# Kernel tuning notes

Measured on AMD Instinct MI355X. Metric: run time of the kernel, lower is better.

The kernel has to match this reference:

```python
import jax, jax.numpy as jnp
import numpy as np

EPS = 1e-5

def _graph_conv(x, src, dst, W, b, N):
    # DGL GraphConv, norm='both': D_out^{-1/2} then aggregate then D_in^{-1/2}
    ones = jnp.ones((src.shape[0],), x.dtype)
    out_deg = jnp.clip(jax.ops.segment_sum(ones, src, num_segments=N), 1.0)
    in_deg = jnp.clip(jax.ops.segment_sum(ones, dst, num_segments=N), 1.0)
    h = (x * (out_deg ** -0.5)[:, None]) @ W          # [N, out] (mult W before gather)
    agg = jax.ops.segment_sum(h[src], dst, num_segments=N)  # [N, out] irregular scatter
    return agg * (in_deg ** -0.5)[:, None] + b

def _bn_relu(h, gamma, beta):
    # BatchNorm1d in training mode: batch stats over node axis (biased var)
    mu = jnp.mean(h, axis=0)
    var = jnp.mean((h - mu) ** 2, axis=0)
    return jax.nn.relu((h - mu) * jax.lax.rsqrt(var + EPS) * gamma + beta)

def setup_inputs() -> dict:
    key = jax.random.key(0)
    ks = jax.random.split(key, 6)
    N, E, F, H, C = 100000, 1000000, 128, 128, 16
    return {
        "x": jax.random.normal(ks[0], (N, F), dtype=jnp.float32),
        "src": jax.random.randint(ks[1], (E,), 0, N, dtype=jnp.int32),
        "dst": jax.random.randint(ks[2], (E,), 0, N, dtype=jnp.int32),
        "W1": jax.random.normal(ks[3], (F, H), dtype=jnp.float32) * 0.05,
        "b1": jnp.zeros((H,), jnp.float32),
        "g1": jnp.ones((H,), jnp.float32),
        "be1": jnp.zeros((H,), jnp.float32),
        "W2": jax.random.normal(ks[4], (H, H), dtype=jnp.float32) * 0.05,
        "b2": jnp.zeros((H,), jnp.float32),
        "g2": jnp.ones((H,), jnp.float32),
        "be2": jnp.zeros((H,), jnp.float32),
        "Wc": jax.random.normal(ks[5], (H, C), dtype=jnp.float32) * 0.05,
        "bc": jnp.zeros((C,), jnp.float32),
    }

def reference(x, src, dst, W1, b1, g1, be1, W2, b2, g2, be2, Wc, bc):
    N = x.shape[0]
    h = _bn_relu(_graph_conv(x, src, dst, W1, b1, N), g1, be1)  # dropout = identity (eval)
    h = _bn_relu(_graph_conv(h, src, dst, W2, b2, N), g2, be2)
    return h @ Wc + bc  # [N, num_cls]
```

## Files before the change

kernel.cpp:

```cpp
#include <hip/hip_runtime.h>

#define FDIM 128
#define MAXDEG 64
#define GATHERB 2048
#define NREP 32

#define RSIZE 128
#define RSHIFT 7
#define RCAP 1024
#define CCAP 14336
#define PCAP 80
#define WCONVB 8

typedef unsigned short ushort_t;
typedef unsigned int uint_t;
typedef __attribute__((ext_vector_type(8))) short short8;
typedef __attribute__((ext_vector_type(16))) float float16;

__device__ __forceinline__ float bflo(uint_t u) { return __uint_as_float(u << 16); }
__device__ __forceinline__ float bfhi(uint_t u) { return __uint_as_float(u & 0xffff0000u); }
__device__ __forceinline__ ushort_t f2bf(float f) {
    uint_t u = __float_as_uint(f);
    return (ushort_t)((u + 0x7fffu + ((u >> 16) & 1u)) >> 16);
}
__device__ __forceinline__ uint_t pack2bf(float lo, float hi) {
    return (uint_t)f2bf(lo) | ((uint_t)f2bf(hi) << 16);
}

__global__ __launch_bounds__(256) void gemm1_kernel(
    const float* __restrict__ x, const ushort_t* __restrict__ wb,
    ushort_t* __restrict__ outb, int N) {
    __shared__ ushort_t zt[64][136];
    __shared__ ushort_t wt[128][136];
    int t = threadIdx.x;
    int base = blockIdx.x * 64;

    const uint4* wb4 = (const uint4*)wb;
    for (int i = t; i < FDIM * 16; i += 256) {
        int n = i >> 4, q = i & 15;
        *(uint4*)&wt[n][q * 8] = wb4[n * 16 + q];
    }
    const float4* x4 = (const float4*)x;
    for (int i = t; i < 64 * 32; i += 256) {
        int row = i >> 5, c4 = i & 31;
        int grow = base + row;
        uint2 o = make_uint2(0u, 0u);
        if (grow < N) {
            float4 v = x4[(size_t)grow * 32 + c4];
            o.x = pack2bf(v.x, v.y);
            o.y = pack2bf(v.z, v.w);
        }
        *(uint2*)&zt[row][c4 * 4] = o;
    }
    __syncthreads();

    int wv = t >> 6, lane = t & 63;
    int rt = wv >> 1;
    int m = lane & 31;
    int kg = lane >> 5;

    short8 af[8];
#pragma unroll
    for (int kk = 0; kk < 8; kk++)
        af[kk] = *(const short8*)&zt[rt * 32 + m][kk * 16 + kg * 8];

#pragma unroll
    for (int cc = 0; cc < 2; cc++) {
        int ct = (wv & 1) * 2 + cc;
        float16 acc = {0, 0, 0, 0, 0, 0, 0, 0, 0, 0, 0, 0, 0, 0, 0, 0};
#pragma unroll
        for (int kk = 0; kk < 8; kk++) {
            short8 bf = *(const short8*)&wt[ct * 32 + m][kk * 16 + kg * 8];
            acc = __builtin_amdgcn_mfma_f32_32x32x16_bf16(af[kk], bf, acc, 0, 0, 0);
        }
        int col = ct * 32 + m;
#pragma unroll
        for (int r = 0; r < 16; r++) {
            int row = base + rt * 32 + (r & 3) + 8 * (r >> 2) + 4 * kg;
            if (row < N) outb[(size_t)row * FDIM + col] = f2bf(acc[r]);
        }
    }
}

__global__ __launch_bounds__(256) void bucket_kernel(
    const int* __restrict__ src, const int* __restrict__ dst,
    uint_t* __restrict__ bktD, int* __restrict__ baseD,
    uint_t* __restrict__ bktS, int* __restrict__ baseS,
    const float* __restrict__ W1, const float* __restrict__ W2,
    ushort_t* __restrict__ wb1, ushort_t* __restrict__ wb2,
    int E, int P, int R) {
    __shared__ uint4 buf4[CCAP / 4];
    __shared__ int hist[RCAP];
    __shared__ int scanbuf[256];
    uint_t* buf = (uint_t*)buf4;
    int t = threadIdx.x;

    if (blockIdx.x >= 2 * P) {
        int t0 = (blockIdx.x - 2 * P) * 256 + t;
        for (int i = t0; i < FDIM * FDIM; i += WCONVB * 256) {
            int k = i >> 7, n = i & 127;
            wb1[n * FDIM + k] = f2bf(W1[i]);
            wb2[n * FDIM + k] = f2bf(W2[i]);
        }
        return;
    }

    int role = blockIdx.x >= P;
    int p = role ? blockIdx.x - P : blockIdx.x;
    const int* key = role ? src : dst;
    int e0 = p * CCAP;
    int e1 = min(E, e0 + CCAP);
    int cnt = e1 - e0;

    for (int r = t; r < R; r += 256) hist[r] = 0;
    __syncthreads();
    for (int i = e0 + t; i < e1; i += 256) atomicAdd(&hist[key[i] >> RSHIFT], 1);
    __syncthreads();

    int b0 = t * 4;
    int hv[4];
    int s0 = 0;
#pragma unroll
    for (int k = 0; k < 4; k++) {
        hv[k] = (b0 + k < R) ? hist[b0 + k] : 0;
        s0 += hv[k];
    }
    scanbuf[t] = s0;
    __syncthreads();
    for (int off = 1; off < 256; off <<= 1) {
        int v = (t >= off) ? scanbuf[t - off] : 0;
        __syncthreads();
        scanbuf[t] += v;
        __syncthreads();
    }
    int run = scanbuf[t] - s0;
    int* baseG = role ? baseS : baseD;
#pragma unroll
    for (int k = 0; k < 4; k++) {
        if (b0 + k < R) {
            baseG[(b0 + k) * P + p] = run;
            hist[b0 + k] = run;
        }
        run += hv[k];
    }
    if (t == 0) baseG[R * P + p] = cnt;
    __syncthreads();

    for (int i = e0 + t; i < e1; i += 256) {
        int kv = key[i];
        int slot = atomicAdd(&hist[kv >> RSHIFT], 1);
        uint_t entry = role ? (uint_t)kv
                            : (((uint_t)(kv & (RSIZE - 1)) << 25) | (uint_t)src[i]);
        buf[slot] = entry;
    }
    __syncthreads();

    uint_t* outp = role ? bktS : bktD;
    uint4* og = (uint4*)(outp + (size_t)e0);
    int n4 = (cnt + 3) >> 2;
    for (int j = t; j < n4; j += 256) og[j] = buf4[j];
}

__global__ __launch_bounds__(256) void build_kernel(
    const uint_t* __restrict__ bktD, const int* __restrict__ baseD,
    const uint_t* __restrict__ bktS, const int* __restrict__ baseS,
    int* __restrict__ eidx, int* __restrict__ cnt, int* __restrict__ cs,
    int N, int P) {
    __shared__ uint4 ell4[RSIZE][MAXDEG / 4];
    __shared__ int cntN[RSIZE], csN[RSIZE];
    __shared__ int dB0[PCAP], dB1[PCAP], sB0[PCAP], sB1[PCAP];
    uint_t* ell = (uint_t*)ell4;
    int t = threadIdx.x;
    int r = blockIdx.x;

    if (t < RSIZE) { cntN[t] = 0; csN[t] = 0; }
    for (int i = t; i < P; i += 256) {
        dB0[i] = baseD[r * P + i];
        dB1[i] = baseD[(r + 1) * P + i];
        sB0[i] = baseS[r * P + i];
        sB1[i] = baseS[(r + 1) * P + i];
    }
    __syncthreads();

    int wave = t >> 6, lane = t & 63;
    for (int p = wave; p < P; p += 4) {
        int b = dB0[p], len = dB1[p] - b;
        const uint_t* seg = bktD + (size_t)p * CCAP + b;
        for (int i = lane; i < len; i += 64) {
            uint_t e = seg[i];
            int dl = e >> 25;
            uint_t s = e & 0x1FFFFFFu;
            int slot = atomicAdd(&cntN[dl], 1);
            if (slot < MAXDEG) ell[dl * MAXDEG + slot] = s;
        }
        int b2 = sB0[p], len2 = sB1[p] - b2;
        const uint_t* seg2 = bktS + (size_t)p * CCAP + b2;
        for (int i = lane; i < len2; i += 64)
            atomicAdd(&csN[seg2[i] & (RSIZE - 1)], 1);
    }
    __syncthreads();

    int base = r * RSIZE;
    for (int i = t; i < RSIZE * (MAXDEG / 4); i += 256) {
        int n = i >> 4, q = i & 15;
        int g = base + n;
        if (g < N && q * 4 < min(cntN[n], MAXDEG))
            ((uint4*)eidx)[(size_t)g * (MAXDEG / 4) + q] = ell4[n][q];
    }
    if (t < RSIZE) {
        int g = base + t;
        if (g < N) { cnt[g] = cntN[t]; cs[g] = csN[t]; }
    }
}

template <bool OS>
__global__ __launch_bounds__(256) void gather_kernel(const ushort_t* __restrict__ hb,
                                                     const int* __restrict__ eidx,
                                                     const int* __restrict__ cnt,
                                                     const int* __restrict__ cs,
                                                     const float* __restrict__ b,
                                                     ushort_t* __restrict__ outb,
                                                     float* __restrict__ statsRep, int N) {
    __shared__ float4 redS[256];
    __shared__ float4 redQ[256];
    int t = threadIdx.x;
    int wave = t >> 6, lane = t & 63;
    int half = lane >> 5, sub = lane & 31;
    int gw = blockIdx.x * 4 + wave;
    const uint2* h2 = (const uint2*)hb;
    uint2* o2 = (uint2*)outb;
    float4 bb = ((const float4*)b)[sub];
    float st0 = 0, st1 = 0, st2 = 0, st3 = 0, sq0 = 0, sq1 = 0, sq2 = 0, sq3 = 0;

    for (int node = gw; node < N; node += GATHERB * 4) {
        int deg = cnt[node];
        int e = min(deg, MAXDEG);
        const int* row = eidx + (size_t)node * MAXDEG;
        int ridx = (lane < e) ? row[lane] : 0;
        float scv = 1.f;
        if (OS) scv = (lane < e) ? rsqrtf((float)max(cs[ridx], 1)) : 0.f;

        float a0 = 0, a1 = 0, a2 = 0, a3 = 0;
        float c0 = 0, c1 = 0, c2 = 0, c3 = 0;
        int j = 0;
        for (; j + 3 < e; j += 4) {
            int iA = __shfl(ridx, j + half);
            int iB = __shfl(ridx, j + 2 + half);
            float sA = OS ? __shfl(scv, j + half) : 1.f;
            float sB = OS ? __shfl(scv, j + 2 + half) : 1.f;
            uint2 uA = h2[(size_t)iA * 32 + sub];
            uint2 uB = h2[(size_t)iB * 32 + sub];
            a0 = fmaf(bflo(uA.x), sA, a0); a1 = fmaf(bfhi(uA.x), sA, a1);
            a2 = fmaf(bflo(uA.y), sA, a2); a3 = fmaf(bfhi(uA.y), sA, a3);
            c0 = fmaf(bflo(uB.x), sB, c0); c1 = fmaf(bfhi(uB.x), sB, c1);
            c2 = fmaf(bflo(uB.y), sB, c2); c3 = fmaf(bfhi(uB.y), sB, c3);
        }
        for (; j < e; j += 2) {
            int jj = j + half;
            bool take = jj < e;
            int i0 = __shfl(ridx, take ? jj : (e - 1));
            float s0 = take ? (OS ? __shfl(scv, jj) : 1.f) : 0.f;
            uint2 u = h2[(size_t)i0 * 32 + sub];
            a0 = fmaf(bflo(u.x), s0, a0); a1 = fmaf(bfhi(u.x), s0, a1);
            a2 = fmaf(bflo(u.y), s0, a2); a3 = fmaf(bfhi(u.y), s0, a3);
        }
        a0 += c0; a1 += c1; a2 += c2; a3 += c3;
        a0 += __shfl_xor(a0, 32);
        a1 += __shfl_xor(a1, 32);
        a2 += __shfl_xor(a2, 32);
        a3 += __shfl_xor(a3, 32);
        if (half == 0) {
            float isc = rsqrtf((float)max(deg, 1));
            uint2 o;
            o.x = pack2bf(fmaf(a0, isc, bb.x), fmaf(a1, isc, bb.y));
            o.y = pack2bf(fmaf(a2, isc, bb.z), fmaf(a3, isc, bb.w));
            o2[(size_t)node * 32 + sub] = o;
            float v0 = bflo(o.x), v1 = bfhi(o.x), v2 = bflo(o.y), v3 = bfhi(o.y);
            st0 += v0; st1 += v1; st2 += v2; st3 += v3;
            sq0 = fmaf(v0, v0, sq0); sq1 = fmaf(v1, v1, sq1);
            sq2 = fmaf(v2, v2, sq2); sq3 = fmaf(v3, v3, sq3);
        }
    }

    redS[t] = make_float4(st0, st1, st2, st3);
    redQ[t] = make_float4(sq0, sq1, sq2, sq3);
    __syncthreads();
    if (t < 32) {
        float4 s = make_float4(0, 0, 0, 0), q = make_float4(0, 0, 0, 0);
#pragma unroll
        for (int w = 0; w < 4; w++) {
            float4 a = redS[w * 64 + t];
            float4 z = redQ[w * 64 + t];
            s.x += a.x; s.y += a.y; s.z += a.z; s.w += a.w;
            q.x += z.x; q.y += z.y; q.z += z.z; q.w += z.w;
        }
        float* dstp = statsRep + (size_t)(blockIdx.x & (NREP - 1)) * 256;
        atomicAdd(&dstp[t * 4 + 0], s.x);
        atomicAdd(&dstp[t * 4 + 1], s.y);
        atomicAdd(&dstp[t * 4 + 2], s.z);
        atomicAdd(&dstp[t * 4 + 3], s.w);
        atomicAdd(&dstp[128 + t * 4 + 0], q.x);
        atomicAdd(&dstp[128 + t * 4 + 1], q.y);
        atomicAdd(&dstp[128 + t * 4 + 2], q.z);
        atomicAdd(&dstp[128 + t * 4 + 3], q.w);
    }
}

__global__ __launch_bounds__(256) void gemm2_kernel(const ushort_t* __restrict__ hb,
                                                    const ushort_t* __restrict__ wb,
                                                    const int* __restrict__ cs,
                                                    const float* __restrict__ statsRep,
                                                    const float* __restrict__ g,
                                                    const float* __restrict__ be,
                                                    ushort_t* __restrict__ outb, int N,
                                                    float invN) {
    __shared__ ushort_t zt[64][136];
    __shared__ ushort_t wt[128][136];
    __shared__ float Ash[FDIM], Bsh[FDIM];
    int t = threadIdx.x;
    int base = blockIdx.x * 64;

    if (t < FDIM) {
        float s = 0.f, q = 0.f;
        for (int r = 0; r < NREP; r++) {
            s += statsRep[r * 256 + t];
            q += statsRep[r * 256 + 128 + t];
        }
        float mu = s * invN;
        float var = q * invN - mu * mu;
        float a = g[t] * rsqrtf(var + 1e-5f);
        Ash[t] = a;
        Bsh[t] = be[t] - mu * a;
    }
    const uint4* wb4 = (const uint4*)wb;
    for (int i = t; i < FDIM * 16; i += 256) {
        int n = i >> 4, q = i & 15;
        *(uint4*)&wt[n][q * 8] = wb4[n * 16 + q];
    }
    __syncthreads();

    const uint_t* h1 = (const uint_t*)hb;
    for (int i = t; i < 64 * 64; i += 256) {
        int row = i >> 6, cp = i & 63;
        int grow = base + row;
        uint_t o = 0;
        if (grow < N) {
            uint_t u = h1[(size_t)grow * 64 + cp];
            float s = rsqrtf((float)max(cs[grow], 1));
            float v0 = fmaxf(fmaf(bflo(u), Ash[cp * 2], Bsh[cp * 2]), 0.f) * s;
            float v1 = fmaxf(fmaf(bfhi(u), Ash[cp * 2 + 1], Bsh[cp * 2 + 1]), 0.f) * s;
            o = pack2bf(v0, v1);
        }
        *(uint_t*)&zt[row][cp * 2] = o;
    }
    __syncthreads();

    int wv = t >> 6, lane = t & 63;
    int rt = wv >> 1;
    int m = lane & 31;
    int kg = lane >> 5;

    short8 af[8];
#pragma unroll
    for (int kk = 0; kk < 8; kk++)
        af[kk] = *(const short8*)&zt[rt * 32 + m][kk * 16 + kg * 8];

#pragma unroll
    for (int cc = 0; cc < 2; cc++) {
        int ct = (wv & 1) * 2 + cc;
        float16 acc = {0, 0, 0, 0, 0, 0, 0, 0, 0, 0, 0, 0, 0, 0, 0, 0};
#pragma unroll
        for (int kk = 0; kk < 8; kk++) {
            short8 bf = *(const short8*)&wt[ct * 32 + m][kk * 16 + kg * 8];
            acc = __builtin_amdgcn_mfma_f32_32x32x16_bf16(af[kk], bf, acc, 0, 0, 0);
        }
        int col = ct * 32 + m;
#pragma unroll
        for (int r = 0; r < 16; r++) {
            int row = base + rt * 32 + (r & 3) + 8 * (r >> 2) + 4 * kg;
            if (row < N) outb[(size_t)row * FDIM + col] = f2bf(acc[r]);
        }
    }
}

__global__ __launch_bounds__(256) void cls_kernel(const ushort_t* __restrict__ hb,
                                                  const float* __restrict__ Wc,
                                                  const float* __restrict__ bc,
                                                  const float* __restrict__ statsRep,
                                                  const float* __restrict__ g,
                                                  const float* __restrict__ be,
                                                  float* __restrict__ out, int N, float invN) {
    __shared__ float wcl[FDIM * 16];
    __shared__ float red[16][256];
    __shared__ float Ash[FDIM], Bsh[FDIM];
    int t = threadIdx.x;
    int base = blockIdx.x * 64;
#pragma unroll
    for (int i = 0; i < 8; i++) wcl[t + i * 256] = Wc[t + i * 256];
    if (t < FDIM) {
        float s = 0.f, q = 0.f;
        for (int r = 0; r < NREP; r++) {
            s += statsRep[r * 256 + t];
            q += statsRep[r * 256 + 128 + t];
        }
        float mu = s * invN;
        float var = q * invN - mu * mu;
        float a = g[t] * rsqrtf(var + 1e-5f);
        Ash[t] = a;
        Bsh[t] = be[t] - mu * a;
    }
    __syncthreads();

    int node = base + (t >> 2);
    int q4 = t & 3;
    float acc[16];
#pragma unroll
    for (int c = 0; c < 16; c++) acc[c] = 0.f;

    if (node < N) {
        const uint2* hu2 = (const uint2*)((const uint_t*)hb + (size_t)node * 64 + q4 * 16);
        const float* Af = Ash + q4 * 32;
        const float* Bf = Bsh + q4 * 32;
#pragma unroll 1
        for (int kk = 0; kk < 8; kk++) {
            uint2 u = hu2[kk];
            float4 ab = *(const float4*)&Af[kk * 4];
            float4 bb = *(const float4*)&Bf[kk * 4];
            float v0 = fmaxf(fmaf(bflo(u.x), ab.x, bb.x), 0.f);
            float v1 = fmaxf(fmaf(bfhi(u.x), ab.y, bb.y), 0.f);
            float v2 = fmaxf(fmaf(bflo(u.y), ab.z, bb.z), 0.f);
            float v3 = fmaxf(fmaf(bfhi(u.y), ab.w, bb.w), 0.f);
            int k0 = q4 * 32 + kk * 4;
            const float* w0 = &wcl[k0 * 16];
#pragma unroll
            for (int c = 0; c < 16; c++) {
                float s = fmaf(v0, w0[c], fmaf(v1, w0[16 + c], fmaf(v2, w0[32 + c], v3 * w0[48 + c])));
                acc[c] += s;
            }
        }
    }
#pragma unroll
    for (int c = 0; c < 16; c++) red[c][t] = acc[c];
    __syncthreads();
#pragma unroll
    for (int i = t; i < 64 * 16; i += 256) {
        int n = i >> 4, c = i & 15;
        float4 p = *(const float4*)&red[c][n * 4];
        int grow = base + n;
        if (grow < N) out[(size_t)grow * 16 + c] = (p.x + p.y) + (p.z + p.w) + bc[c];
    }
}

extern "C" void kernel_launch(void* const* d_in, const int* in_sizes, int n_in,
                              void* d_out, int out_size, void* d_ws, size_t ws_size,
                              hipStream_t stream) {
    const float* x  = (const float*)d_in[0];
    const int* src  = (const int*)d_in[1];
    const int* dst  = (const int*)d_in[2];
    const float* W1 = (const float*)d_in[3];
    const float* b1 = (const float*)d_in[4];
    const float* g1 = (const float*)d_in[5];
    const float* be1= (const float*)d_in[6];
    const float* W2 = (const float*)d_in[7];
    const float* b2 = (const float*)d_in[8];
    const float* g2 = (const float*)d_in[9];
    const float* be2= (const float*)d_in[10];
    const float* Wc = (const float*)d_in[11];
    const float* bc = (const float*)d_in[12];
    float* out = (float*)d_out;

    int N = in_sizes[0] / FDIM;
    int E = in_sizes[1];
    size_t NB = (size_t)N * FDIM;

    ushort_t* bufA = (ushort_t*)d_ws;
    ushort_t* bufB = bufA + NB;
    int* cs        = (int*)(bufB + NB);
    int* cnt       = cs + N;
    float* statsR1 = (float*)(cnt + N);
    float* statsR2 = statsR1 + NREP * 256;
    int* eidx      = (int*)(statsR2 + NREP * 256);
    ushort_t* wb1  = (ushort_t*)(eidx + (size_t)N * MAXDEG);
    ushort_t* wb2  = wb1 + FDIM * FDIM;

    uint_t* bktD = (uint_t*)bufB;
    uint_t* bktS = bktD + (size_t)PCAP * CCAP;
    int* baseD   = (int*)(bktS + (size_t)PCAP * CCAP);
    int* baseS   = baseD + (RCAP + 1) * PCAP;

    int P = (E + CCAP - 1) / CCAP;
    int R = (N + RSIZE - 1) >> RSHIFT;

    hipMemsetAsync(statsR1, 0, (size_t)2 * NREP * 256 * sizeof(float), stream);

    bucket_kernel<<<2 * P + WCONVB, 256, 0, stream>>>(
        src, dst, bktD, baseD, bktS, baseS, W1, W2, wb1, wb2, E, P, R);
    build_kernel<<<R, 256, 0, stream>>>(bktD, baseD, bktS, baseS, eidx, cnt, cs, N, P);

    gemm1_kernel<<<(N + 63) / 64, 256, 0, stream>>>(x, wb1, bufA, N);

    float invN = 1.0f / N;

    gather_kernel<true><<<GATHERB, 256, 0, stream>>>(bufA, eidx, cnt, cs, b1, bufB, statsR1, N);

    gemm2_kernel<<<(N + 63) / 64, 256, 0, stream>>>(bufB, wb2, cs, statsR1, g1, be1, bufA, N, invN);
    gather_kernel<false><<<GATHERB, 256, 0, stream>>>(bufA, eidx, cnt, nullptr, b2, bufB, statsR2, N);

    cls_kernel<<<(N + 63) / 64, 256, 0, stream>>>(bufB, Wc, bc, statsR2, g2, be2, out, N, invN);
}
```

Measured before the change: 347.2 us.

## Fold out-degree scaling into gemm1 epilogue and prefetch/unroll gather loop

The source-side D_out^-1/2 scaling for layer 1 moves into the gemm1 epilogue, where each row is scaled by rsqrt(out-degree) before the bf16 store. This removes the per-edge cs lookup, rsqrt and scale shuffles from the first gather. The gather kernel now loads the next node's degree and neighbor indices one iteration ahead, and adds an 8-wide unrolled inner loop so more row loads are in flight. The gemm1 change alters bf16 rounding order slightly. Indices are now read unconditionally for all 64 lanes, which depends on padded eidx rows being valid.

```diff
diff --git a/kernel.cpp b/kernel.cpp
--- a/kernel.cpp
+++ b/kernel.cpp
@@ -29,9 +29,11 @@
 
 __global__ __launch_bounds__(256) void gemm1_kernel(
     const float* __restrict__ x, const ushort_t* __restrict__ wb,
+    const int* __restrict__ cs,
     ushort_t* __restrict__ outb, int N) {
     __shared__ ushort_t zt[64][136];
     __shared__ ushort_t wt[128][136];
+    __shared__ float csh[64];
     int t = threadIdx.x;
     int base = blockIdx.x * 64;
 
@@ -39,6 +41,10 @@
     for (int i = t; i < FDIM * 16; i += 256) {
         int n = i >> 4, q = i & 15;
         *(uint4*)&wt[n][q * 8] = wb4[n * 16 + q];
+    }
+    if (t < 64) {
+        int g = base + t;
+        csh[t] = (g < N) ? rsqrtf((float)max(cs[g], 1)) : 1.f;
     }
     const float4* x4 = (const float4*)x;
     for (int i = t; i < 64 * 32; i += 256) {
@@ -76,8 +82,9 @@
         int col = ct * 32 + m;
 #pragma unroll
         for (int r = 0; r < 16; r++) {
-            int row = base + rt * 32 + (r & 3) + 8 * (r >> 2) + 4 * kg;
-            if (row < N) outb[(size_t)row * FDIM + col] = f2bf(acc[r]);
+            int rl = rt * 32 + (r & 3) + 8 * (r >> 2) + 4 * kg;
+            int row = base + rl;
+            if (row < N) outb[(size_t)row * FDIM + col] = f2bf(acc[r] * csh[rl]);
         }
     }
 }
@@ -213,11 +220,9 @@
     }
 }
 
-template <bool OS>
 __global__ __launch_bounds__(256) void gather_kernel(const ushort_t* __restrict__ hb,
                                                      const int* __restrict__ eidx,
                                                      const int* __restrict__ cnt,
-                                                     const int* __restrict__ cs,
                                                      const float* __restrict__ b,
                                                      ushort_t* __restrict__ outb,
                                                      float* __restrict__ statsRep, int N) {
@@ -226,43 +231,61 @@
     int t = threadIdx.x;
     int wave = t >> 6, lane = t & 63;
     int half = lane >> 5, sub = lane & 31;
+    const int STRIDE = GATHERB * 4;
     int gw = blockIdx.x * 4 + wave;
     const uint2* h2 = (const uint2*)hb;
     uint2* o2 = (uint2*)outb;
     float4 bb = ((const float4*)b)[sub];
     float st0 = 0, st1 = 0, st2 = 0, st3 = 0, sq0 = 0, sq1 = 0, sq2 = 0, sq3 = 0;
 
-    for (int node = gw; node < N; node += GATHERB * 4) {
-        int deg = cnt[node];
+    int node = gw;
+    int deg = 0, ridx = 0;
+    if (node < N) {
+        deg = cnt[node];
+        ridx = eidx[(size_t)node * MAXDEG + lane];
+    }
+    while (node < N) {
+        int nnode = node + STRIDE;
+        int ndeg = 0, nridx = 0;
+        if (nnode < N) {
+            ndeg = cnt[nnode];
+            nridx = eidx[(size_t)nnode * MAXDEG + lane];
+        }
+
         int e = min(deg, MAXDEG);
-        const int* row = eidx + (size_t)node * MAXDEG;
-        int ridx = (lane < e) ? row[lane] : 0;
-        float scv = 1.f;
-        if (OS) scv = (lane < e) ? rsqrtf((float)max(cs[ridx], 1)) : 0.f;
-
         float a0 = 0, a1 = 0, a2 = 0, a3 = 0;
         float c0 = 0, c1 = 0, c2 = 0, c3 = 0;
         int j = 0;
+        for (; j + 7 < e; j += 8) {
+            int iA = __shfl(ridx, j + half);
+            int iB = __shfl(ridx, j + 2 + half);
+            int iC = __shfl(ridx, j + 4 + half);
+            int iD = __shfl(ridx, j + 6 + half);
+            uint2 uA = h2[(size_t)iA * 32 + sub];
+            uint2 uB = h2[(size_t)iB * 32 + sub];
+            uint2 uC = h2[(size_t)iC * 32 + sub];
+            uint2 uD = h2[(size_t)iD * 32 + sub];
+            a0 += bflo(uA.x); a1 += bfhi(uA.x); a2 += bflo(uA.y); a3 += bfhi(uA.y);
+            c0 += bflo(uB.x); c1 += bfhi(uB.x); c2 += bflo(uB.y); c3 += bfhi(uB.y);
+            a0 += bflo(uC.x); a1 += bfhi(uC.x); a2 += bflo(uC.y); a3 += bfhi(uC.y);
+            c0 += bflo(uD.x); c1 += bfhi(uD.x); c2 += bflo(uD.y); c3 += bfhi(uD.y);
+        }
         for (; j + 3 < e; j += 4) {
             int iA = __shfl(ridx, j + half);
             int iB = __shfl(ridx, j + 2 + half);
-            float sA = OS ? __shfl(scv, j + half) : 1.f;
-            float sB = OS ? __shfl(scv, j + 2 + half) : 1.f;
             uint2 uA = h2[(size_t)iA * 32 + sub];
             uint2 uB = h2[(size_t)iB * 32 + sub];
-            a0 = fmaf(bflo(uA.x), sA, a0); a1 = fmaf(bfhi(uA.x), sA, a1);
-            a2 = fmaf(bflo(uA.y), sA, a2); a3 = fmaf(bfhi(uA.y), sA, a3);
-            c0 = fmaf(bflo(uB.x), sB, c0); c1 = fmaf(bfhi(uB.x), sB, c1);
-            c2 = fmaf(bflo(uB.y), sB, c2); c3 = fmaf(bfhi(uB.y), sB, c3);
+            a0 += bflo(uA.x); a1 += bfhi(uA.x); a2 += bflo(uA.y); a3 += bfhi(uA.y);
+            c0 += bflo(uB.x); c1 += bfhi(uB.x); c2 += bflo(uB.y); c3 += bfhi(uB.y);
         }
         for (; j < e; j += 2) {
             int jj = j + half;
             bool take = jj < e;
             int i0 = __shfl(ridx, take ? jj : (e - 1));
-            float s0 = take ? (OS ? __shfl(scv, jj) : 1.f) : 0.f;
+            float m = take ? 1.f : 0.f;
             uint2 u = h2[(size_t)i0 * 32 + sub];
-            a0 = fmaf(bflo(u.x), s0, a0); a1 = fmaf(bfhi(u.x), s0, a1);
-            a2 = fmaf(bflo(u.y), s0, a2); a3 = fmaf(bfhi(u.y), s0, a3);
+            a0 = fmaf(bflo(u.x), m, a0); a1 = fmaf(bfhi(u.x), m, a1);
+            a2 = fmaf(bflo(u.y), m, a2); a3 = fmaf(bfhi(u.y), m, a3);
         }
         a0 += c0; a1 += c1; a2 += c2; a3 += c3;
         a0 += __shfl_xor(a0, 32);
@@ -280,6 +303,7 @@
             sq0 = fmaf(v0, v0, sq0); sq1 = fmaf(v1, v1, sq1);
             sq2 = fmaf(v2, v2, sq2); sq3 = fmaf(v3, v3, sq3);
         }
+        node = nnode; deg = ndeg; ridx = nridx;
     }
 
     redS[t] = make_float4(st0, st1, st2, st3);
@@ -497,14 +521,14 @@
         src, dst, bktD, baseD, bktS, baseS, W1, W2, wb1, wb2, E, P, R);
     build_kernel<<<R, 256, 0, stream>>>(bktD, baseD, bktS, baseS, eidx, cnt, cs, N, P);
 
-    gemm1_kernel<<<(N + 63) / 64, 256, 0, stream>>>(x, wb1, bufA, N);
+    gemm1_kernel<<<(N + 63) / 64, 256, 0, stream>>>(x, wb1, cs, bufA, N);
 
     float invN = 1.0f / N;
 
-    gather_kernel<true><<<GATHERB, 256, 0, stream>>>(bufA, eidx, cnt, cs, b1, bufB, statsR1, N);
+    gather_kernel<<<GATHERB, 256, 0, stream>>>(bufA, eidx, cnt, b1, bufB, statsR1, N);
 
     gemm2_kernel<<<(N + 63) / 64, 256, 0, stream>>>(bufB, wb2, cs, statsR1, g1, be1, bufA, N, invN);
-    gather_kernel<false><<<GATHERB, 256, 0, stream>>>(bufA, eidx, cnt, nullptr, b2, bufB, statsR2, N);
+    gather_kernel<<<GATHERB, 256, 0, stream>>>(bufA, eidx, cnt, b2, bufB, statsR2, N);
 
     cls_kernel<<<(N + 63) / 64, 256, 0, stream>>>(bufB, Wc, bc, statsR2, g2, be2, out, N, invN);
 }
```

New measurement: 351.2 us. Within noise of the previous version (+1.2%).
